# Performance work log

Hardware: AMD Instinct MI355X
Metric: run time of the kernel (lower is better)

The kernel has to match this reference:

```python
import jax, jax.numpy as jnp
import numpy as np

VOCAB, EMBED, HIDDEN = 32000, 512, 1024
B, T = 8, 256

def setup_inputs() -> dict:
    key = jax.random.key(0)
    ks = jax.random.split(key, 5)
    x = jax.random.randint(ks[0], (B, T), 0, VOCAB)
    embedding = jax.random.normal(ks[1], (VOCAB, EMBED), dtype=jnp.float32)
    W_xh = jax.random.normal(ks[2], (EMBED, HIDDEN), dtype=jnp.float32) * 0.01
    W_hh = jax.random.normal(ks[3], (HIDDEN, HIDDEN), dtype=jnp.float32) * 0.01
    b_h = jnp.zeros((HIDDEN,), dtype=jnp.float32)
    W_hy = jax.random.normal(ks[4], (HIDDEN, VOCAB), dtype=jnp.float32) * 0.01
    b_y = jnp.zeros((VOCAB,), dtype=jnp.float32)
    return {"x": x, "embedding": embedding, "W_xh": W_xh, "W_hh": W_hh,
            "b_h": b_h, "W_hy": W_hy, "b_y": b_y}

def reference(x, embedding, W_xh, W_hh, b_h, W_hy, b_y):
    # x: [B,T] int ids
    emb = embedding[x]                      # [B,T,E]
    # Precompute input contribution for all steps: [B,T,H]
    xh = jnp.einsum('bte,eh->bth', emb, W_xh) + b_h
    h0 = jnp.zeros((x.shape[0], W_hh.shape[0]), dtype=emb.dtype)

    def step(h, xh_t):
        h = jnp.tanh(xh_t + h @ W_hh)       # [B,H]
        return h, h

    _, hs = jax.lax.scan(step, h0, jnp.swapaxes(xh, 0, 1))  # hs: [T,B,H]
    hs = jnp.swapaxes(hs, 0, 1)             # [B,T,H]
    # Output projection batched over all timesteps (same math as per-step)
    y = jnp.einsum('bth,hv->btv', hs, W_hy) + b_y  # [B,T,V]
    return y
```

## Files before the change

### kernel.cpp

```cpp
#include <hip/hip_runtime.h>
#include <hip/hip_bf16.h>

#define VOCAB 32000
#define EMBED 512
#define HIDDEN 1024
#define NB 8
#define NT 256
#define XH_ROWS 16

#define NCH 8
#define NMEM 32
#define RCOLS 32

typedef __attribute__((ext_vector_type(8))) short bf16x8;
typedef __attribute__((ext_vector_type(4))) float f32x4;
typedef __attribute__((ext_vector_type(4))) unsigned u32x4;

#define AS1 __attribute__((address_space(1)))
#define AS3 __attribute__((address_space(3)))

__device__ __forceinline__ unsigned short bf16_bits(float f) {
    __hip_bfloat16 b = __float2bfloat16(f);
    unsigned short s;
    __builtin_memcpy(&s, &b, 2);
    return s;
}
__device__ __forceinline__ float lo16f(unsigned u) { return __uint_as_float(u << 16); }
__device__ __forceinline__ float hi16f(unsigned u) { return __uint_as_float(u & 0xffff0000u); }

__global__ __launch_bounds__(256) void k_transpose(const float* __restrict__ W,
                                                   __hip_bfloat16* __restrict__ Wt) {
    __shared__ float tile[32][33];
    const int n0 = blockIdx.x * 32;
    const int k0 = blockIdx.y * 32;
    const int c = threadIdx.x & 31;
    const int r0 = threadIdx.x >> 5;
#pragma unroll
    for (int rr = 0; rr < 4; ++rr) {
        const int r = r0 + rr * 8;
        tile[c][r] = W[(size_t)(k0 + r) * VOCAB + n0 + c];
    }
    __syncthreads();
#pragma unroll
    for (int rr = 0; rr < 4; ++rr) {
        const int n = r0 + rr * 8;
        Wt[(size_t)(n0 + n) * HIDDEN + k0 + c] = __float2bfloat16(tile[n][c]);
    }
}

__global__ __launch_bounds__(256) void k_xh(const int* __restrict__ ids,
                                            const float* __restrict__ emb,
                                            const float* __restrict__ Wxh,
                                            const float* __restrict__ bh,
                                            float* __restrict__ xh) {
    __shared__ alignas(16) float embS[XH_ROWS][EMBED];
    __shared__ int idsS[XH_ROWS];
    const int tid = threadIdx.x;
    const int blk = blockIdx.x;
    if (tid < XH_ROWS) idsS[tid] = ids[blk * XH_ROWS + tid];
    __syncthreads();
    const float4* emb4 = (const float4*)emb;
#pragma unroll
    for (int rep = 0; rep < (XH_ROWS * EMBED / 4) / 256; ++rep) {
        const int lin = rep * 256 + tid;
        const int r = lin >> 7;
        const int e4 = lin & 127;
        *(float4*)&embS[r][e4 * 4] = emb4[(size_t)idsS[r] * (EMBED / 4) + e4];
    }
    __syncthreads();
    float4 acc[XH_ROWS] = {};
    const float4* W4 = (const float4*)Wxh;
    for (int e = 0; e < EMBED; ++e) {
        const float4 w = W4[(size_t)e * (HIDDEN / 4) + tid];
#pragma unroll
        for (int r = 0; r < XH_ROWS; ++r) {
            const float ev = embS[r][e];
            acc[r].x += ev * w.x; acc[r].y += ev * w.y;
            acc[r].z += ev * w.z; acc[r].w += ev * w.w;
        }
    }
    const float4 bv = ((const float4*)bh)[tid];
#pragma unroll
    for (int r = 0; r < XH_ROWS; ++r) {
        float4 o;
        o.x = acc[r].x + bv.x; o.y = acc[r].y + bv.y;
        o.z = acc[r].z + bv.z; o.w = acc[r].w + bv.w;
        ((float4*)xh)[(size_t)(blk * XH_ROWS + r) * (HIDDEN / 4) + tid] = o;
    }
}

__global__ __launch_bounds__(256, 1) void k_rec(const float* __restrict__ Whh,
                                                const float* __restrict__ xh,
                                                unsigned long long* __restrict__ hx,
                                                __hip_bfloat16* __restrict__ hs) {
    __shared__ float xhS[NT * RCOLS];
    __shared__ float hS[16 * 68];
    __shared__ float red[16 * 33];
    const int tid = threadIdx.x;
    const int bid = blockIdx.x;
    const int c = bid & (NCH - 1);
    const int m = bid >> 3;
    const int j0 = m * RCOLS;
    unsigned long long* hxc = hx + (size_t)c * 1024;

    if (tid < 16)
        __hip_atomic_store(&hxc[512 + m * 16 + tid], 0ull, __ATOMIC_RELAXED,
                           __HIP_MEMORY_SCOPE_AGENT);

    const int col2 = tid & 15;
    const int part = tid >> 4;

    u32x4 wreg[16];
#pragma unroll
    for (int j = 0; j < 16; ++j) {
        u32x4 q;
#pragma unroll
        for (int e = 0; e < 4; ++e) {
            const int i = part * 64 + 4 * j + e;
            const float2 wv = *(const float2*)&Whh[(size_t)i * HIDDEN + j0 + 2 * col2];
            q[e] = (unsigned)bf16_bits(wv.x) | ((unsigned)bf16_bits(wv.y) << 16);
        }
        wreg[j] = q;
    }
    for (int idx = tid; idx < NT * RCOLS; idx += 256) {
        const int t = idx >> 5;
        const int col = idx & 31;
        xhS[idx] = xh[(size_t)(c * NT + t) * HIDDEN + j0 + col];
    }
    __syncthreads();

    const f32x4* hv4 = (const f32x4*)&hS[part * 68];
    const int w0 = tid;
    const int w1 = tid + 256;
    const int pe0 = 2 * tid + 4 * (tid >> 5);

    for (int t = 0; t < NT; ++t) {
        unsigned long long* rbuf = hxc + ((t + 1) & 1) * 512;
        unsigned long long* wbuf = hxc + (t & 1) * 512;
        const unsigned long long tok = (unsigned long long)(unsigned)t;
        unsigned long long a = __hip_atomic_load(&rbuf[w0], __ATOMIC_RELAXED, __HIP_MEMORY_SCOPE_AGENT);
        unsigned long long b = __hip_atomic_load(&rbuf[w1], __ATOMIC_RELAXED, __HIP_MEMORY_SCOPE_AGENT);
        while (((a & 0xffffull) != tok) | ((b & 0xffffull) != tok)) {
            __builtin_amdgcn_s_sleep(1);
            if ((a & 0xffffull) != tok)
                a = __hip_atomic_load(&rbuf[w0], __ATOMIC_RELAXED, __HIP_MEMORY_SCOPE_AGENT);
            if ((b & 0xffffull) != tok)
                b = __hip_atomic_load(&rbuf[w1], __ATOMIC_RELAXED, __HIP_MEMORY_SCOPE_AGENT);
        }
        *(float2*)&hS[pe0] = make_float2(__uint_as_float(((unsigned)(a >> 16) & 0xffffu) << 16),
                                         __uint_as_float(((unsigned)(a >> 32) & 0xffffu) << 16));
        *(float2*)&hS[pe0 + 544] = make_float2(__uint_as_float(((unsigned)(b >> 16) & 0xffffu) << 16),
                                               __uint_as_float(((unsigned)(b >> 32) & 0xffffu) << 16));
        __syncthreads();
        float a0 = 0.f, a1 = 0.f;
#pragma unroll
        for (int j = 0; j < 16; ++j) {
            const u32x4 w4 = wreg[j];
            const f32x4 h4 = hv4[j];
            a0 = fmaf(lo16f(w4.x), h4.x, a0); a1 = fmaf(hi16f(w4.x), h4.x, a1);
            a0 = fmaf(lo16f(w4.y), h4.y, a0); a1 = fmaf(hi16f(w4.y), h4.y, a1);
            a0 = fmaf(lo16f(w4.z), h4.z, a0); a1 = fmaf(hi16f(w4.z), h4.z, a1);
            a0 = fmaf(lo16f(w4.w), h4.w, a0); a1 = fmaf(hi16f(w4.w), h4.w, a1);
        }
        red[part * 33 + 2 * col2]     = a0;
        red[part * 33 + 2 * col2 + 1] = a1;
        __syncthreads();
        if (tid < RCOLS) {
            float s = 0.f;
#pragma unroll
            for (int p = 0; p < 16; ++p) s += red[p * 33 + tid];
            const float v = tanhf(xhS[t * RCOLS + tid] + s);
            const unsigned hb = (unsigned)bf16_bits(v);
            ((unsigned short*)hs)[(size_t)(c * NT + t) * HIDDEN + j0 + tid] = (unsigned short)hb;
            const unsigned pb = (unsigned)__shfl_xor((int)hb, 1, 64);
            if ((tid & 1) == 0) {
                const unsigned long long wv = (unsigned long long)(unsigned)(t + 1)
                                            | ((unsigned long long)hb << 16)
                                            | ((unsigned long long)pb << 32);
                __hip_atomic_store(&wbuf[m * 16 + (tid >> 1)], wv, __ATOMIC_RELAXED,
                                   __HIP_MEMORY_SCOPE_AGENT);
            }
        }
    }
}

__global__ __launch_bounds__(512, 2) void k_proj(const unsigned short* __restrict__ A,
                                                 const unsigned short* __restrict__ Bt,
                                                 const float* __restrict__ by,
                                                 float* __restrict__ C) {
    __shared__ unsigned short LDS[4][16384];
    const int tid = threadIdx.x;
    const int wid = tid >> 6;
    const int lane = tid & 63;
    const int lin = blockIdx.x;
    const int swz = (lin & 7) * 125 + (lin >> 3);
    const int mt = swz & 7, nt = swz >> 3;
    const int m0 = mt * 256, n0 = nt * 256;
    const int wr = wid >> 2, wc = wid & 3;
    const int fr = lane & 15, fq = lane >> 4;
    const int srow = tid >> 3;
    const int sslot = tid & 7;

    f32x4 acc[8][4] = {};

#define STAGE(kt, bf)                                                                     \
    {                                                                                     \
        const unsigned short* Ag = A + (size_t)m0 * HIDDEN + (size_t)(kt) * 64;           \
        const unsigned short* Bg = Bt + (size_t)n0 * HIDDEN + (size_t)(kt) * 64;          \
        _Pragma("unroll")                                                                 \
        for (int j = 0; j < 4; ++j) {                                                     \
            const int r = j * 64 + srow;                                                  \
            const int ls = ((sslot ^ (r & 7)) * 8);                                       \
            __builtin_amdgcn_global_load_lds(                                             \
                (const AS1 unsigned*)(Ag + (size_t)r * HIDDEN + ls),                      \
                (AS3 unsigned*)(&LDS[(bf) * 2 + 0][j * 4096 + wid * 512]), 16, 0, 0);     \
        }                                                                                 \
        _Pragma("unroll")                                                                 \
        for (int j = 0; j < 4; ++j) {                                                     \
            const int r = j * 64 + srow;                                                  \
            const int ls = ((sslot ^ (r & 7)) * 8);                                       \
            __builtin_amdgcn_global_load_lds(                                             \
                (const AS1 unsigned*)(Bg + (size_t)r * HIDDEN + ls),                      \
                (AS3 unsigned*)(&LDS[(bf) * 2 + 1][j * 4096 + wid * 512]), 16, 0, 0);     \
        }                                                                                 \
    }

    STAGE(0, 0);
    STAGE(1, 1);

    int cur = 0;
    for (int kt = 0; kt < 16; ++kt) {
        if (kt < 15) { asm volatile("s_waitcnt vmcnt(8)" ::: "memory"); }
        else         { asm volatile("s_waitcnt vmcnt(0)" ::: "memory"); }
        __builtin_amdgcn_s_barrier();

        const unsigned short* Ab = &LDS[cur * 2 + 0][0];
        const unsigned short* Bb = &LDS[cur * 2 + 1][0];
        bf16x8 af[8][2], bg[4][2];
#pragma unroll
        for (int mi = 0; mi < 8; ++mi) {
            const int ra = wr * 128 + mi * 16 + fr;
#pragma unroll
            for (int ks = 0; ks < 2; ++ks)
                af[mi][ks] = *(const bf16x8*)&Ab[ra * 64 + (((ks * 4 + fq) ^ (fr & 7)) * 8)];
        }
#pragma unroll
        for (int ni = 0; ni < 4; ++ni) {
            const int rb = wc * 64 + ni * 16 + fr;
#pragma unroll
            for (int ks = 0; ks < 2; ++ks)
                bg[ni][ks] = *(const bf16x8*)&Bb[rb * 64 + (((ks * 4 + fq) ^ (fr & 7)) * 8)];
        }
        asm volatile("s_waitcnt lgkmcnt(0)" ::: "memory");
        __builtin_amdgcn_sched_barrier(0);
        __builtin_amdgcn_s_barrier();

        if (kt < 14) STAGE(kt + 2, cur);

        __builtin_amdgcn_s_setprio(1);
#pragma unroll
        for (int mi = 0; mi < 8; ++mi)
#pragma unroll
            for (int ni = 0; ni < 4; ++ni) {
                acc[mi][ni] = __builtin_amdgcn_mfma_f32_16x16x32_bf16(af[mi][0], bg[ni][0], acc[mi][ni], 0, 0, 0);
                acc[mi][ni] = __builtin_amdgcn_mfma_f32_16x16x32_bf16(af[mi][1], bg[ni][1], acc[mi][ni], 0, 0, 0);
            }
        __builtin_amdgcn_s_setprio(0);
        cur ^= 1;
    }
#undef STAGE

#pragma unroll
    for (int ni = 0; ni < 4; ++ni) {
        const int col = n0 + wc * 64 + ni * 16 + fr;
        const float bias = by[col];
#pragma unroll
        for (int mi = 0; mi < 8; ++mi) {
            const int row = m0 + wr * 128 + mi * 16 + fq * 4;
            float* cp = C + (size_t)row * VOCAB + col;
            cp[0]                 = acc[mi][ni][0] + bias;
            cp[(size_t)VOCAB]     = acc[mi][ni][1] + bias;
            cp[(size_t)2 * VOCAB] = acc[mi][ni][2] + bias;
            cp[(size_t)3 * VOCAB] = acc[mi][ni][3] + bias;
        }
    }
}

extern "C" void kernel_launch(void* const* d_in, const int* in_sizes, int n_in,
                              void* d_out, int out_size, void* d_ws, size_t ws_size,
                              hipStream_t stream) {
    const int*   x   = (const int*)d_in[0];
    const float* emb = (const float*)d_in[1];
    const float* Wxh = (const float*)d_in[2];
    const float* Whh = (const float*)d_in[3];
    const float* bh  = (const float*)d_in[4];
    const float* Why = (const float*)d_in[5];
    const float* by  = (const float*)d_in[6];
    float* y = (float*)d_out;

    char* ws = (char*)d_ws;
    const size_t off_xh = 0;
    const size_t off_hx = off_xh + (size_t)NB * NT * HIDDEN * 4;
    const size_t off_hs = off_hx + (size_t)NCH * 2 * 512 * 8;
    const size_t off_wt = off_hs + (size_t)NB * NT * HIDDEN * 2;
    const size_t need   = off_wt + (size_t)VOCAB * HIDDEN * 2;
    if (ws_size < need) return;

    float* xh = (float*)(ws + off_xh);
    unsigned long long* hx = (unsigned long long*)(ws + off_hx);
    __hip_bfloat16* hs = (__hip_bfloat16*)(ws + off_hs);
    __hip_bfloat16* Wt = (__hip_bfloat16*)(ws + off_wt);

    k_xh<<<dim3((NB * NT) / XH_ROWS), 256, 0, stream>>>(x, emb, Wxh, bh, xh);
    k_transpose<<<dim3(VOCAB / 32, HIDDEN / 32), 256, 0, stream>>>(Why, Wt);
    k_rec<<<dim3(NCH * NMEM), 256, 0, stream>>>(Whh, xh, hx, hs);
    k_proj<<<dim3((2048 / 256) * (VOCAB / 256)), 512, 0, stream>>>((const unsigned short*)hs,
                                                                   (const unsigned short*)Wt, by, y);
}
```

Baseline: 803.7 us.

## Pin recurrence chains to XCDs and poll a fast L2-local handoff buffer

Each recurrence block reads its hardware XCD id and claims a chain and member slot through atomic counters, so all 32 blocks of one batch chain run on the same XCD. Blocks that find their XCD already full wait until every block has arrived, then take the leftover slots. The hidden-state handoff is now written twice: once with agent scope and once with workgroup scope into a second buffer. Polling reads the second buffer with sc0 loads that can be served from the XCD-local L2, and only sometimes falls back to the agent-scope buffer. This is meant to cut cross-XCD coherence latency on the serial per-step exchange, at the cost of an extra memset, slot-assignment overhead and reliance on undocumented cache-scope behaviour.

After: 965.2 us. +20.1%, slower.

```diff
diff --git a/kernel.cpp b/kernel.cpp
--- a/kernel.cpp
+++ b/kernel.cpp
@@ -27,6 +27,21 @@
 }
 __device__ __forceinline__ float lo16f(unsigned u) { return __uint_as_float(u << 16); }
 __device__ __forceinline__ float hi16f(unsigned u) { return __uint_as_float(u & 0xffff0000u); }
+
+__device__ __forceinline__ unsigned long long sc0_load64(const unsigned long long* p) {
+    unsigned long long v;
+    asm volatile("global_load_dwordx2 %0, %1, off sc0\n\ts_waitcnt vmcnt(0)"
+                 : "=v"(v) : "v"(p) : "memory");
+    return v;
+}
+__device__ __forceinline__ void sc0_load64x2(unsigned long long& a, unsigned long long& b,
+                                             const unsigned long long* p0,
+                                             const unsigned long long* p1) {
+    asm volatile("global_load_dwordx2 %0, %2, off sc0\n\t"
+                 "global_load_dwordx2 %1, %3, off sc0\n\t"
+                 "s_waitcnt vmcnt(0)"
+                 : "=&v"(a), "=&v"(b) : "v"(p0), "v"(p1) : "memory");
+}
 
 __global__ __launch_bounds__(256) void k_transpose(const float* __restrict__ W,
                                                    __hip_bfloat16* __restrict__ Wt) {
@@ -91,21 +106,56 @@
 
 __global__ __launch_bounds__(256, 1) void k_rec(const float* __restrict__ Whh,
                                                 const float* __restrict__ xh,
-                                                unsigned long long* __restrict__ hx,
+                                                unsigned long long* __restrict__ hxA,
+                                                unsigned long long* __restrict__ hxF,
+                                                unsigned* __restrict__ ctr,
                                                 __hip_bfloat16* __restrict__ hs) {
     __shared__ float xhS[NT * RCOLS];
     __shared__ float hS[16 * 68];
     __shared__ float red[16 * 33];
+    __shared__ int sChain, sMember;
     const int tid = threadIdx.x;
-    const int bid = blockIdx.x;
-    const int c = bid & (NCH - 1);
-    const int m = bid >> 3;
+
+    if (tid == 0) {
+        unsigned xcd;
+        asm volatile("s_getreg_b32 %0, hwreg(20, 0, 4)" : "=s"(xcd));
+        xcd &= 7u;
+        const unsigned slot = __hip_atomic_fetch_add(&ctr[xcd], 1u, __ATOMIC_RELAXED,
+                                                     __HIP_MEMORY_SCOPE_AGENT);
+        __hip_atomic_fetch_add(&ctr[8], 1u, __ATOMIC_ACQ_REL, __HIP_MEMORY_SCOPE_AGENT);
+        int chain, member;
+        if (slot < (unsigned)NMEM) {
+            chain = (int)xcd; member = (int)slot;
+        } else {
+            while (__hip_atomic_load(&ctr[8], __ATOMIC_ACQUIRE, __HIP_MEMORY_SCOPE_AGENT) < 256u)
+                __builtin_amdgcn_s_sleep(2);
+            const unsigned oidx = __hip_atomic_fetch_add(&ctr[9], 1u, __ATOMIC_RELAXED,
+                                                         __HIP_MEMORY_SCOPE_AGENT);
+            int k = -1; chain = 0; member = 0;
+            for (int c2 = 0; c2 < 8 && k < (int)oidx; ++c2) {
+                unsigned cf = __hip_atomic_load(&ctr[c2], __ATOMIC_RELAXED, __HIP_MEMORY_SCOPE_AGENT);
+                int filled = cf < (unsigned)NMEM ? (int)cf : NMEM;
+                for (int m2 = filled; m2 < NMEM && k < (int)oidx; ++m2) {
+                    ++k;
+                    if (k == (int)oidx) { chain = c2; member = m2; }
+                }
+            }
+        }
+        sChain = chain; sMember = member;
+    }
+    __syncthreads();
+    const int c = sChain;
+    const int m = sMember;
     const int j0 = m * RCOLS;
-    unsigned long long* hxc = hx + (size_t)c * 1024;
-
-    if (tid < 16)
-        __hip_atomic_store(&hxc[512 + m * 16 + tid], 0ull, __ATOMIC_RELAXED,
+    unsigned long long* hxcA = hxA + (size_t)c * 1024;
+    unsigned long long* hxcF = hxF + (size_t)c * 1024;
+
+    if (tid < 16) {
+        __hip_atomic_store(&hxcA[512 + m * 16 + tid], 0ull, __ATOMIC_RELAXED,
                            __HIP_MEMORY_SCOPE_AGENT);
+        __hip_atomic_store(&hxcF[512 + m * 16 + tid], 0ull, __ATOMIC_RELAXED,
+                           __HIP_MEMORY_SCOPE_WORKGROUP);
+    }
 
     const int col2 = tid & 15;
     const int part = tid >> 4;
@@ -135,17 +185,25 @@
     const int pe0 = 2 * tid + 4 * (tid >> 5);
 
     for (int t = 0; t < NT; ++t) {
-        unsigned long long* rbuf = hxc + ((t + 1) & 1) * 512;
-        unsigned long long* wbuf = hxc + (t & 1) * 512;
+        const int roff = ((t + 1) & 1) * 512;
+        const int woff = (t & 1) * 512;
         const unsigned long long tok = (unsigned long long)(unsigned)t;
-        unsigned long long a = __hip_atomic_load(&rbuf[w0], __ATOMIC_RELAXED, __HIP_MEMORY_SCOPE_AGENT);
-        unsigned long long b = __hip_atomic_load(&rbuf[w1], __ATOMIC_RELAXED, __HIP_MEMORY_SCOPE_AGENT);
+        const unsigned long long* pF0 = hxcF + roff + w0;
+        const unsigned long long* pF1 = hxcF + roff + w1;
+        const unsigned long long* pA0 = hxcA + roff + w0;
+        const unsigned long long* pA1 = hxcA + roff + w1;
+        unsigned long long a, b;
+        sc0_load64x2(a, b, pF0, pF1);
+        int tries = 0;
         while (((a & 0xffffull) != tok) | ((b & 0xffffull) != tok)) {
-            __builtin_amdgcn_s_sleep(1);
+            ++tries;
+            const bool useFast = (tries <= 3) | ((tries & 1) != 0);
             if ((a & 0xffffull) != tok)
-                a = __hip_atomic_load(&rbuf[w0], __ATOMIC_RELAXED, __HIP_MEMORY_SCOPE_AGENT);
+                a = useFast ? sc0_load64(pF0)
+                            : __hip_atomic_load(pA0, __ATOMIC_RELAXED, __HIP_MEMORY_SCOPE_AGENT);
             if ((b & 0xffffull) != tok)
-                b = __hip_atomic_load(&rbuf[w1], __ATOMIC_RELAXED, __HIP_MEMORY_SCOPE_AGENT);
+                b = useFast ? sc0_load64(pF1)
+                            : __hip_atomic_load(pA1, __ATOMIC_RELAXED, __HIP_MEMORY_SCOPE_AGENT);
         }
         *(float2*)&hS[pe0] = make_float2(__uint_as_float(((unsigned)(a >> 16) & 0xffffu) << 16),
                                          __uint_as_float(((unsigned)(a >> 32) & 0xffffu) << 16));
@@ -177,8 +235,10 @@
                 const unsigned long long wv = (unsigned long long)(unsigned)(t + 1)
                                             | ((unsigned long long)hb << 16)
                                             | ((unsigned long long)pb << 32);
-                __hip_atomic_store(&wbuf[m * 16 + (tid >> 1)], wv, __ATOMIC_RELAXED,
+                __hip_atomic_store(&hxcA[woff + m * 16 + (tid >> 1)], wv, __ATOMIC_RELAXED,
                                    __HIP_MEMORY_SCOPE_AGENT);
+                __hip_atomic_store(&hxcF[woff + m * 16 + (tid >> 1)], wv, __ATOMIC_RELAXED,
+                                   __HIP_MEMORY_SCOPE_WORKGROUP);
             }
         }
     }
@@ -299,21 +359,26 @@
     float* y = (float*)d_out;
 
     char* ws = (char*)d_ws;
-    const size_t off_xh = 0;
-    const size_t off_hx = off_xh + (size_t)NB * NT * HIDDEN * 4;
-    const size_t off_hs = off_hx + (size_t)NCH * 2 * 512 * 8;
-    const size_t off_wt = off_hs + (size_t)NB * NT * HIDDEN * 2;
-    const size_t need   = off_wt + (size_t)VOCAB * HIDDEN * 2;
+    const size_t off_xh  = 0;
+    const size_t off_hxa = off_xh + (size_t)NB * NT * HIDDEN * 4;
+    const size_t off_hxf = off_hxa + (size_t)NCH * 2 * 512 * 8;
+    const size_t off_ctr = off_hxf + (size_t)NCH * 2 * 512 * 8;
+    const size_t off_hs  = off_ctr + 256;
+    const size_t off_wt  = off_hs + (size_t)NB * NT * HIDDEN * 2;
+    const size_t need    = off_wt + (size_t)VOCAB * HIDDEN * 2;
     if (ws_size < need) return;
 
     float* xh = (float*)(ws + off_xh);
-    unsigned long long* hx = (unsigned long long*)(ws + off_hx);
+    unsigned long long* hxA = (unsigned long long*)(ws + off_hxa);
+    unsigned long long* hxF = (unsigned long long*)(ws + off_hxf);
+    unsigned* ctr = (unsigned*)(ws + off_ctr);
     __hip_bfloat16* hs = (__hip_bfloat16*)(ws + off_hs);
     __hip_bfloat16* Wt = (__hip_bfloat16*)(ws + off_wt);
 
+    hipMemsetAsync(ctr, 0, 256, stream);
     k_xh<<<dim3((NB * NT) / XH_ROWS), 256, 0, stream>>>(x, emb, Wxh, bh, xh);
     k_transpose<<<dim3(VOCAB / 32, HIDDEN / 32), 256, 0, stream>>>(Why, Wt);
-    k_rec<<<dim3(NCH * NMEM), 256, 0, stream>>>(Whh, xh, hx, hs);
+    k_rec<<<dim3(NCH * NMEM), 256, 0, stream>>>(Whh, xh, hxA, hxF, ctr, hs);
     k_proj<<<dim3((2048 / 256) * (VOCAB / 256)), 512, 0, stream>>>((const unsigned short*)hs,
                                                                    (const unsigned short*)Wt, by, y);
 }
```

## Overlap W_hy transpose with recurrence by adding extra blocks to fused kernel

Applied to the files above, without the earlier changes.

Removes the standalone transpose kernel and appends 64 extra blocks to the recurrence launch that each transpose and bf16-convert 500 tiles of W_hy, reusing the recurrence's shared memory buffer. The aim is to hide the transpose's memory traffic behind the latency-bound recurrence, which uses only 256 blocks. The risk is that the extra blocks compete with the recurrence blocks for memory bandwidth and CUs. If the recurrence relies on all its blocks being co-resident for its cross-block spin synchronisation, the extra blocks could also affect scheduling.

After: 798.8 us. Within noise of the previous version (-0.6%).

```diff
diff --git a/kernel.cpp b/kernel.cpp
--- a/kernel.cpp
+++ b/kernel.cpp
@@ -11,6 +11,9 @@
 #define NCH 8
 #define NMEM 32
 #define RCOLS 32
+#define NBLK_REC 256
+#define NBLK_TR 64
+#define TILES_PER_TR 500
 
 typedef __attribute__((ext_vector_type(8))) short bf16x8;
 typedef __attribute__((ext_vector_type(4))) float f32x4;
@@ -27,26 +30,6 @@
 }
 __device__ __forceinline__ float lo16f(unsigned u) { return __uint_as_float(u << 16); }
 __device__ __forceinline__ float hi16f(unsigned u) { return __uint_as_float(u & 0xffff0000u); }
-
-__global__ __launch_bounds__(256) void k_transpose(const float* __restrict__ W,
-                                                   __hip_bfloat16* __restrict__ Wt) {
-    __shared__ float tile[32][33];
-    const int n0 = blockIdx.x * 32;
-    const int k0 = blockIdx.y * 32;
-    const int c = threadIdx.x & 31;
-    const int r0 = threadIdx.x >> 5;
-#pragma unroll
-    for (int rr = 0; rr < 4; ++rr) {
-        const int r = r0 + rr * 8;
-        tile[c][r] = W[(size_t)(k0 + r) * VOCAB + n0 + c];
-    }
-    __syncthreads();
-#pragma unroll
-    for (int rr = 0; rr < 4; ++rr) {
-        const int n = r0 + rr * 8;
-        Wt[(size_t)(n0 + n) * HIDDEN + k0 + c] = __float2bfloat16(tile[n][c]);
-    }
-}
 
 __global__ __launch_bounds__(256) void k_xh(const int* __restrict__ ids,
                                             const float* __restrict__ emb,
@@ -89,15 +72,43 @@
     }
 }
 
-__global__ __launch_bounds__(256, 1) void k_rec(const float* __restrict__ Whh,
-                                                const float* __restrict__ xh,
-                                                unsigned long long* __restrict__ hx,
-                                                __hip_bfloat16* __restrict__ hs) {
+__global__ __launch_bounds__(256, 1) void k_fused(const float* __restrict__ Whh,
+                                                  const float* __restrict__ xh,
+                                                  unsigned long long* __restrict__ hx,
+                                                  __hip_bfloat16* __restrict__ hs,
+                                                  const float* __restrict__ Why,
+                                                  __hip_bfloat16* __restrict__ Wt) {
     __shared__ float xhS[NT * RCOLS];
     __shared__ float hS[16 * 68];
     __shared__ float red[16 * 33];
     const int tid = threadIdx.x;
     const int bid = blockIdx.x;
+
+    if (bid >= NBLK_REC) {
+        const int tb = bid - NBLK_REC;
+        float (*tile)[33] = (float(*)[33])xhS;
+        const int cc = tid & 31;
+        const int r0 = tid >> 5;
+        for (int i = 0; i < TILES_PER_TR; ++i) {
+            const int g = tb * TILES_PER_TR + i;
+            const int n0 = (g % 1000) * 32;
+            const int k0 = (g / 1000) * 32;
+            __syncthreads();
+#pragma unroll
+            for (int rr = 0; rr < 4; ++rr) {
+                const int r = r0 + rr * 8;
+                tile[cc][r] = Why[(size_t)(k0 + r) * VOCAB + n0 + cc];
+            }
+            __syncthreads();
+#pragma unroll
+            for (int rr = 0; rr < 4; ++rr) {
+                const int n = r0 + rr * 8;
+                Wt[(size_t)(n0 + n) * HIDDEN + k0 + cc] = __float2bfloat16(tile[n][cc]);
+            }
+        }
+        return;
+    }
+
     const int c = bid & (NCH - 1);
     const int m = bid >> 3;
     const int j0 = m * RCOLS;
@@ -312,8 +323,7 @@
     __hip_bfloat16* Wt = (__hip_bfloat16*)(ws + off_wt);
 
     k_xh<<<dim3((NB * NT) / XH_ROWS), 256, 0, stream>>>(x, emb, Wxh, bh, xh);
-    k_transpose<<<dim3(VOCAB / 32, HIDDEN / 32), 256, 0, stream>>>(Why, Wt);
-    k_rec<<<dim3(NCH * NMEM), 256, 0, stream>>>(Whh, xh, hx, hs);
+    k_fused<<<dim3(NBLK_REC + NBLK_TR), 256, 0, stream>>>(Whh, xh, hx, hs, Why, Wt);
     k_proj<<<dim3((2048 / 256) * (VOCAB / 256)), 512, 0, stream>>>((const unsigned short*)hs,
                                                                    (const unsigned short*)Wt, by, y);
 }
```
